# Kernel optimization log

Hardware: AMD Instinct MI355X
Metric: run time of the kernel (lower is better)

Reference implementation:

```python
import jax, jax.numpy as jnp
import numpy as np

N, E = 100000, 1600000
IN, H, ED, L, OUT = 128, 64, 64, 3, 3

def _lin(key, fan_in, fan_out):
    return jax.random.normal(key, (fan_in, fan_out), jnp.float32) / np.sqrt(fan_in)

def setup_inputs() -> dict:
    key = jax.random.key(0)
    ks = jax.random.split(key, 16)
    x = jax.random.normal(ks[0], (N, IN), jnp.float32)
    edge_index = jax.random.randint(ks[1], (2, E), 0, N, dtype=jnp.int64)
    edge_attr = jax.random.normal(ks[2], (E, ED), jnp.float32)
    pW = _lin(ks[3], IN, H); pb = jnp.zeros((H,), jnp.float32)
    # stacked per-layer params
    eW1 = jnp.stack([_lin(jax.random.fold_in(ks[4], l), 2 * H + ED, ED) for l in range(L)])
    eb1 = jnp.zeros((L, ED), jnp.float32)
    eW2 = jnp.stack([_lin(jax.random.fold_in(ks[5], l), ED, ED) for l in range(L)])
    eb2 = jnp.zeros((L, ED), jnp.float32)
    nW1 = jnp.stack([_lin(jax.random.fold_in(ks[6], l), H + ED, H) for l in range(L)])
    nb1 = jnp.zeros((L, H), jnp.float32)
    nW2 = jnp.stack([_lin(jax.random.fold_in(ks[7], l), H, H) for l in range(L)])
    nb2 = jnp.zeros((L, H), jnp.float32)
    lW = _lin(ks[8], H, OUT); lb = jnp.zeros((OUT,), jnp.float32)
    return {"x": x, "edge_index": edge_index, "edge_attr": edge_attr,
            "pW": pW, "pb": pb, "eW1": eW1, "eb1": eb1, "eW2": eW2, "eb2": eb2,
            "nW1": nW1, "nb1": nb1, "nW2": nW2, "nb2": nb2, "lW": lW, "lb": lb}

def reference(x, edge_index, edge_attr, pW, pb, eW1, eb1, eW2, eb2, nW1, nb1, nW2, nb2, lW, lb):
    n = x.shape[0]
    row, col = edge_index[0], edge_index[1]  # source j, target i
    h = x @ pW + pb                          # node_proj
    ea = edge_attr
    for l in range(eW1.shape[0]):
        # edge_mlp([x_row, x_col, e])
        ein = jnp.concatenate([h[row], h[col], ea], axis=-1)        # [E, 2H+ED]
        ea = jax.nn.relu(ein @ eW1[l] + eb1[l]) @ eW2[l] + eb2[l]   # [E, ED]
        # message = node_mlp([x_j, e]) with x_j = h[row]
        mi = jnp.concatenate([h[row], ea], axis=-1)                 # [E, H+ED]
        msg = jax.nn.relu(mi @ nW1[l] + nb1[l]) @ nW2[l] + nb2[l]   # [E, H]
        agg = jax.ops.segment_sum(msg, col, num_segments=n)         # scatter-add into targets
        h = jax.nn.relu(agg + h)                                    # update + outer ReLU (dropout=eval)
    pooled = jnp.mean(h, axis=0, keepdims=True)                     # global_mean_pool, single graph
    return pooled @ lW + lb
```

## Files before the change

### kernel.cpp

```cpp
#include <hip/hip_runtime.h>

#define NN 100000
#define NE 1600000
#define BINS_PAD 100352

typedef short s8v __attribute__((ext_vector_type(8)));
typedef float f32x4 __attribute__((ext_vector_type(4)));
typedef unsigned short u16;

__device__ __forceinline__ u16 f2bf(float f) {
    union { float f; unsigned u; } v; v.f = f;
    unsigned r = v.u + 0x7FFFu + ((v.u >> 16) & 1u);
    return (u16)(r >> 16);
}
__device__ __forceinline__ unsigned pk2(float a, float b) {
    return (unsigned)f2bf(a) | ((unsigned)f2bf(b) << 16);
}

__global__ void pack_weights(const float* __restrict__ pW,
                             const float* __restrict__ eW1, const float* __restrict__ eW2,
                             const float* __restrict__ nW1, const float* __restrict__ nW2,
                             u16* __restrict__ wpack) {
    int b = blockIdx.x, L = threadIdx.x;
    const float* src; int s, t;
    if (b < 16) { src = pW; s = b >> 2; t = b & 3; }
    else {
        int bb = b - 16, l = bb / 56, r = bb % 56;
        if (r < 24)      {            src = eW1 + l*192*64; s = r>>2; t = r&3; }
        else if (r < 32) { r -= 24;   src = eW2 + l*64*64;  s = r>>2; t = r&3; }
        else if (r < 48) { r -= 32;   src = nW1 + l*128*64; s = r>>2; t = r&3; }
        else             { r -= 48;   src = nW2 + l*64*64;  s = r>>2; t = r&3; }
    }
    int kbase = s*32 + (L>>4)*8;
    int n = t*16 + (L&15);
    u16* dst = wpack + (size_t)b*512 + (size_t)L*8;
#pragma unroll
    for (int j = 0; j < 8; ++j) dst[j] = f2bf(src[(kbase+j)*64 + n]);
}

__global__ void k_hist(const int* __restrict__ ei, int* __restrict__ hist) {
    int e = blockIdx.x * 256 + threadIdx.x;
    atomicAdd(&hist[ei[(size_t)NE + e]], 1);
}

__global__ void k_scan1(const int* __restrict__ hist, int* __restrict__ cursor,
                        int* __restrict__ blockSums) {
    __shared__ int sS[256];
    int t = threadIdx.x, b = blockIdx.x;
    int base = b*1024 + t*4;
    int v0 = hist[base], v1 = hist[base+1], v2 = hist[base+2], v3 = hist[base+3];
    int s4 = v0 + v1 + v2 + v3;
    sS[t] = s4; __syncthreads();
    for (int off = 1; off < 256; off <<= 1) {
        int x = (t >= off) ? sS[t-off] : 0;
        __syncthreads();
        sS[t] += x;
        __syncthreads();
    }
    int excl = sS[t] - s4;
    cursor[base] = excl; cursor[base+1] = excl+v0;
    cursor[base+2] = excl+v0+v1; cursor[base+3] = excl+v0+v1+v2;
    if (t == 255) blockSums[b] = sS[255];
}

__global__ void k_scan2(int* __restrict__ blockSums) {
    __shared__ int sS[128];
    int t = threadIdx.x;
    int v = (t < 98) ? blockSums[t] : 0;
    sS[t] = v; __syncthreads();
    for (int off = 1; off < 128; off <<= 1) {
        int x = (t >= off) ? sS[t-off] : 0;
        __syncthreads();
        sS[t] += x;
        __syncthreads();
    }
    if (t < 98) blockSums[t] = sS[t] - v;
}

__global__ void k_scan3(int* __restrict__ cursor, const int* __restrict__ blockSums) {
    int i = blockIdx.x*1024 + threadIdx.x*4;
    int add = blockSums[blockIdx.x];
    cursor[i] += add; cursor[i+1] += add; cursor[i+2] += add; cursor[i+3] += add;
}

__global__ void k_scatter(const int* __restrict__ ei, int* __restrict__ cursor,
                          int* __restrict__ rowP, int* __restrict__ colP,
                          int* __restrict__ pos) {
    int e = blockIdx.x * 256 + threadIdx.x;
    int c = ei[(size_t)NE + e];
    int p = atomicAdd(&cursor[c], 1);
    rowP[p] = ei[e];
    colP[p] = c;
    pos[e] = p;
}

__global__ void k_permute_ea(const float* __restrict__ ea, const int* __restrict__ pos,
                             u16* __restrict__ eaP) {
    int g = threadIdx.x >> 6, lane = threadIdx.x & 63;
    int e = blockIdx.x * 4 + g;
    int p = pos[e];
    eaP[(size_t)p*64 + lane] = f2bf(ea[(size_t)e*64 + lane]);
}

__global__ __launch_bounds__(256) void node_proj(const float* __restrict__ x,
                                                 const float* __restrict__ pb,
                                                 const u16* __restrict__ wpack,
                                                 float* __restrict__ h,
                                                 u16* __restrict__ h_bf) {
    __shared__ __align__(16) u16 sX[64*136];
    const int tid = threadIdx.x;
    const int n0 = blockIdx.x * 64;
    for (int i = tid; i < 64*32; i += 256) {
        int node = i >> 5, c = i & 31;
        float4 v = make_float4(0.f, 0.f, 0.f, 0.f);
        if (n0 + node < NN) v = *(const float4*)(x + (size_t)(n0+node)*128 + c*4);
        *(uint2*)&sX[node*136 + c*4] = make_uint2(pk2(v.x, v.y), pk2(v.z, v.w));
    }
    __syncthreads();
    const int w = tid >> 6, L = tid & 63;
    const int m = L & 15, kc = L >> 4;
    const int wb = w * 16;
    const f32x4 z = {0.f, 0.f, 0.f, 0.f};
    f32x4 acc[4] = {z, z, z, z};
#pragma unroll
    for (int s = 0; s < 4; ++s) {
        s8v a = *(const s8v*)&sX[(wb+m)*136 + s*32 + kc*8];
#pragma unroll
        for (int t = 0; t < 4; ++t) {
            s8v bf = *(const s8v*)(wpack + ((size_t)(s*4+t)*64 + L)*8);
            acc[t] = __builtin_amdgcn_mfma_f32_16x16x32_bf16(a, bf, acc[t], 0, 0, 0);
        }
    }
#pragma unroll
    for (int t = 0; t < 4; ++t) {
        int u = t*16 + m;
        float bias = pb[u];
#pragma unroll
        for (int r = 0; r < 4; ++r) {
            int node = n0 + wb + kc*4 + r;
            if (node < NN) {
                float v = acc[t][r] + bias;
                h[(size_t)node*64 + u] = v;
                h_bf[(size_t)node*64 + u] = f2bf(v);
            }
        }
    }
}

__global__ __launch_bounds__(256, 4) void edge_layer(const int* __restrict__ rowP,
                                                     const int* __restrict__ colP,
                                                     const u16* __restrict__ h_bf,
                                                     u16* __restrict__ ea_bf,
                                                     const u16* __restrict__ wp,
                                                     const float* __restrict__ eb1,
                                                     const float* __restrict__ eb2,
                                                     const float* __restrict__ nb1,
                                                     const float* __restrict__ nb2,
                                                     float* __restrict__ agg) {
    __shared__ __align__(16) u16 sB[4*32*136];
    __shared__ int sColP[128];
    __shared__ int sSeg[130];
    __shared__ int sCnt0, sK;
    float* msg = (float*)sB;
    const int tid = threadIdx.x;
    const int w = tid >> 6, L = tid & 63;
    const int m = L & 15, kc = L >> 4;
    const int wb = w * 32;
    const size_t e0 = (size_t)blockIdx.x * 128;
    u16* sW = sB + w * 32 * 136;

    if (tid < 128) sColP[tid] = colP[e0 + tid];
    __syncthreads();
    bool st = false;
    if (tid < 128) st = (tid == 0) || (sColP[tid] != sColP[tid-1]);
    unsigned long long mask = __ballot(st);
    if (tid == 0) sCnt0 = __popcll(mask);
    __syncthreads();
    if (st) {
        int base = (tid >= 64) ? sCnt0 : 0;
        int idx = base + __popcll(mask & ((1ull << (tid & 63)) - 1ull));
        sSeg[idx] = tid;
    }
    if (tid == 64) { int k = sCnt0 + __popcll(mask); sK = k; sSeg[k] = 128; }

    float be1[4], be2[4], bn1[4], bn2[4];
#pragma unroll
    for (int t = 0; t < 4; ++t) {
        int u = t*16 + m;
        be1[t] = eb1[u]; be2[t] = eb2[u]; bn1[t] = nb1[u]; bn2[t] = nb2[u];
    }
    int rowI[2], colI[2];
#pragma unroll
    for (int g = 0; g < 2; ++g) {
        rowI[g] = rowP[e0 + wb + g*16 + m];
        colI[g] = sColP[wb + g*16 + m];
    }

    const f32x4 z = {0.f, 0.f, 0.f, 0.f};
    f32x4 acc[2][4];

#pragma unroll
    for (int g = 0; g < 2; ++g)
#pragma unroll
        for (int t = 0; t < 4; ++t) acc[g][t] = z;
#pragma unroll
    for (int s = 0; s < 6; ++s) {
        s8v a[2];
#pragma unroll
        for (int g = 0; g < 2; ++g) {
            if (s < 2)
                a[g] = *(const s8v*)(h_bf + (size_t)rowI[g]*64 + s*32 + kc*8);
            else if (s < 4)
                a[g] = *(const s8v*)(h_bf + (size_t)colI[g]*64 + (s-2)*32 + kc*8);
            else
                a[g] = *(const s8v*)(ea_bf + (e0 + wb + g*16 + m)*64 + (s-4)*32 + kc*8);
        }
#pragma unroll
        for (int t = 0; t < 4; ++t) {
            s8v bf = *(const s8v*)(wp + ((size_t)(s*4+t)*64 + L)*8);
            acc[0][t] = __builtin_amdgcn_mfma_f32_16x16x32_bf16(a[0], bf, acc[0][t], 0, 0, 0);
            acc[1][t] = __builtin_amdgcn_mfma_f32_16x16x32_bf16(a[1], bf, acc[1][t], 0, 0, 0);
        }
    }
#pragma unroll
    for (int g = 0; g < 2; ++g)
#pragma unroll
        for (int t = 0; t < 4; ++t) {
            int u = t*16 + m;
#pragma unroll
            for (int r = 0; r < 4; ++r) {
                float v = acc[g][t][r] + be1[t];
                v = v > 0.f ? v : 0.f;
                sW[(g*16 + kc*4 + r)*136 + u] = f2bf(v);
            }
        }

    const u16* wp2 = wp + 24*512;
#pragma unroll
    for (int g = 0; g < 2; ++g)
#pragma unroll
        for (int t = 0; t < 4; ++t) acc[g][t] = z;
#pragma unroll
    for (int s = 0; s < 2; ++s) {
        s8v a0 = *(const s8v*)&sW[(m)*136 + s*32 + kc*8];
        s8v a1 = *(const s8v*)&sW[(16 + m)*136 + s*32 + kc*8];
#pragma unroll
        for (int t = 0; t < 4; ++t) {
            s8v bf = *(const s8v*)(wp2 + ((size_t)(s*4+t)*64 + L)*8);
            acc[0][t] = __builtin_amdgcn_mfma_f32_16x16x32_bf16(a0, bf, acc[0][t], 0, 0, 0);
            acc[1][t] = __builtin_amdgcn_mfma_f32_16x16x32_bf16(a1, bf, acc[1][t], 0, 0, 0);
        }
    }
#pragma unroll
    for (int g = 0; g < 2; ++g)
#pragma unroll
        for (int t = 0; t < 4; ++t) {
            int u = t*16 + m;
#pragma unroll
            for (int r = 0; r < 4; ++r) {
                float v = acc[g][t][r] + be2[t];
                sW[(g*16 + kc*4 + r)*136 + 64 + u] = f2bf(v);
            }
        }

    const u16* wp3 = wp + 32*512;
#pragma unroll
    for (int g = 0; g < 2; ++g)
#pragma unroll
        for (int t = 0; t < 4; ++t) acc[g][t] = z;
#pragma unroll
    for (int s = 0; s < 4; ++s) {
        s8v a[2];
#pragma unroll
        for (int g = 0; g < 2; ++g) {
            if (s < 2) {
                a[g] = *(const s8v*)(h_bf + (size_t)rowI[g]*64 + s*32 + kc*8);
            } else {
                a[g] = *(const s8v*)&sW[(g*16 + m)*136 + 64 + (s-2)*32 + kc*8];
                *(s8v*)(ea_bf + (e0 + wb + g*16 + m)*64 + (s-2)*32 + kc*8) = a[g];
            }
        }
#pragma unroll
        for (int t = 0; t < 4; ++t) {
            s8v bf = *(const s8v*)(wp3 + ((size_t)(s*4+t)*64 + L)*8);
            acc[0][t] = __builtin_amdgcn_mfma_f32_16x16x32_bf16(a[0], bf, acc[0][t], 0, 0, 0);
            acc[1][t] = __builtin_amdgcn_mfma_f32_16x16x32_bf16(a[1], bf, acc[1][t], 0, 0, 0);
        }
    }
#pragma unroll
    for (int g = 0; g < 2; ++g)
#pragma unroll
        for (int t = 0; t < 4; ++t) {
            int u = t*16 + m;
#pragma unroll
            for (int r = 0; r < 4; ++r) {
                float v = acc[g][t][r] + bn1[t];
                v = v > 0.f ? v : 0.f;
                sW[(g*16 + kc*4 + r)*136 + u] = f2bf(v);
            }
        }

    const u16* wp4 = wp + 48*512;
#pragma unroll
    for (int g = 0; g < 2; ++g)
#pragma unroll
        for (int t = 0; t < 4; ++t) acc[g][t] = z;
#pragma unroll
    for (int s = 0; s < 2; ++s) {
        s8v a0 = *(const s8v*)&sW[(m)*136 + s*32 + kc*8];
        s8v a1 = *(const s8v*)&sW[(16 + m)*136 + s*32 + kc*8];
#pragma unroll
        for (int t = 0; t < 4; ++t) {
            s8v bf = *(const s8v*)(wp4 + ((size_t)(s*4+t)*64 + L)*8);
            acc[0][t] = __builtin_amdgcn_mfma_f32_16x16x32_bf16(a0, bf, acc[0][t], 0, 0, 0);
            acc[1][t] = __builtin_amdgcn_mfma_f32_16x16x32_bf16(a1, bf, acc[1][t], 0, 0, 0);
        }
    }

    __syncthreads();
#pragma unroll
    for (int g = 0; g < 2; ++g)
#pragma unroll
        for (int t = 0; t < 4; ++t) {
#pragma unroll
            for (int r = 0; r < 4; ++r) {
                int er = wb + g*16 + kc*4 + r;
                msg[er*66 + t*16 + m] = acc[g][t][r] + bn2[t];
            }
        }
    __syncthreads();

    int k = sK;
    for (int s = w; s < k; s += 4) {
        int beg = sSeg[s], end = sSeg[s+1];
        int node = sColP[beg];
        float sum = 0.f;
        for (int e = beg; e < end; ++e) sum += msg[e*66 + L];
        unsafeAtomicAdd(&agg[(size_t)node*64 + L], sum);
    }
}

__global__ void update_h(float* __restrict__ h, float* __restrict__ agg,
                         u16* __restrict__ h_bf, int zero_agg) {
    int i = (blockIdx.x * 256 + threadIdx.x) * 4;
    float4 a = *(const float4*)(agg + i);
    float4 hv = *(const float4*)(h + i);
    float4 v;
    v.x = fmaxf(a.x + hv.x, 0.f);
    v.y = fmaxf(a.y + hv.y, 0.f);
    v.z = fmaxf(a.z + hv.z, 0.f);
    v.w = fmaxf(a.w + hv.w, 0.f);
    *(float4*)(h + i) = v;
    *(uint2*)(h_bf + i) = make_uint2(pk2(v.x, v.y), pk2(v.z, v.w));
    if (zero_agg) *(float4*)(agg + i) = make_float4(0.f, 0.f, 0.f, 0.f);
}

__global__ void pool1(const float* __restrict__ h, float* __restrict__ pooled) {
    float acc = 0.f;
    const int stride = gridDim.x * 256;
    for (int i = blockIdx.x * 256 + threadIdx.x; i < NN*64; i += stride)
        acc += h[i];
    __shared__ float sp[256];
    sp[threadIdx.x] = acc;
    __syncthreads();
    if (threadIdx.x < 64) {
        float v = sp[threadIdx.x] + sp[threadIdx.x+64] + sp[threadIdx.x+128] + sp[threadIdx.x+192];
        unsafeAtomicAdd(&pooled[threadIdx.x], v);
    }
}

__global__ void pool2(const float* __restrict__ pooled, const float* __restrict__ lW,
                      const float* __restrict__ lb, float* __restrict__ out) {
    int k = threadIdx.x;
    float v = pooled[k] * (1.0f / NN);
#pragma unroll
    for (int o = 0; o < 3; ++o) {
        float p = v * lW[k*3 + o];
        for (int off = 32; off > 0; off >>= 1)
            p += __shfl_down(p, off);
        if (k == 0) out[o] = p + lb[o];
    }
}

extern "C" void kernel_launch(void* const* d_in, const int* in_sizes, int n_in,
                              void* d_out, int out_size, void* d_ws, size_t ws_size,
                              hipStream_t stream) {
    const float* x         = (const float*)d_in[0];
    const int*   ei        = (const int*)d_in[1];
    const float* edge_attr = (const float*)d_in[2];
    const float* pW        = (const float*)d_in[3];
    const float* pb        = (const float*)d_in[4];
    const float* eW1       = (const float*)d_in[5];
    const float* eb1       = (const float*)d_in[6];
    const float* eW2       = (const float*)d_in[7];
    const float* eb2       = (const float*)d_in[8];
    const float* nW1       = (const float*)d_in[9];
    const float* nb1       = (const float*)d_in[10];
    const float* nW2       = (const float*)d_in[11];
    const float* nb2       = (const float*)d_in[12];
    const float* lW        = (const float*)d_in[13];
    const float* lb        = (const float*)d_in[14];
    float* out = (float*)d_out;

    char* ws = (char*)d_ws;
    float* h     = (float*)(ws);
    float* agg   = (float*)(ws + 25600000);
    u16*   h_bf  = (u16*)  (ws + 51200000);
    u16*   eaP   = (u16*)  (ws + 64000000);
    u16*   wpack = (u16*)  (ws + 268800000);
    float* pooled= (float*)(ws + 268988416);
    int*   rowP  = (int*)  (ws + 268988672);
    int*   colP  = (int*)  (ws + 275388672);
    int* hist      = (int*)agg;
    int* cursor    = hist + BINS_PAD;
    int* blockSums = cursor + BINS_PAD;
    int* pos       = blockSums + 128;

    hipMemsetAsync(hist, 0, BINS_PAD*4, stream);
    k_hist<<<NE/256, 256, 0, stream>>>(ei, hist);
    k_scan1<<<98, 256, 0, stream>>>(hist, cursor, blockSums);
    k_scan2<<<1, 128, 0, stream>>>(blockSums);
    k_scan3<<<98, 256, 0, stream>>>(cursor, blockSums);
    k_scatter<<<NE/256, 256, 0, stream>>>(ei, cursor, rowP, colP, pos);
    k_permute_ea<<<NE/4, 256, 0, stream>>>(edge_attr, pos, eaP);

    pack_weights<<<184, 64, 0, stream>>>(pW, eW1, eW2, nW1, nW2, wpack);
    node_proj<<<(NN + 63)/64, 256, 0, stream>>>(x, pb, wpack, h, h_bf);

    hipMemsetAsync(agg, 0, (size_t)NN*64*4, stream);
    for (int l = 0; l < 3; ++l) {
        edge_layer<<<NE/128, 256, 0, stream>>>(rowP, colP, h_bf, eaP,
                                               wpack + (16 + l*56)*512,
                                               eb1 + l*64, eb2 + l*64, nb1 + l*64, nb2 + l*64,
                                               agg);
        update_h<<<NN*64/4/256, 256, 0, stream>>>(h, agg, h_bf, l < 2 ? 1 : 0);
    }
    hipMemsetAsync(pooled, 0, 64*4, stream);
    pool1<<<256, 256, 0, stream>>>(h, pooled);
    pool2<<<1, 64, 0, stream>>>(pooled, lW, lb, out);
}
```

Baseline: 1.731 ms.

## Reduce edge-layer messages in registers with wave shuffles and trim LDS and stores

The edge layer no longer stages messages in shared memory with block-wide segment discovery. Each wave finds its own target-node segments with ballot and shuffle, reduces the MFMA accumulators in registers, and issues the atomics directly. This shrinks the LDS tile stride so occupancy can rise to 6 blocks per SM. It also packs row and col indices into a single int2 array, vectorises the edge-attribute permutation, and skips the edge-attribute and bf16 h writes in the last layer. The cost is more atomics when a target node's edges span several waves, plus a serial per-segment loop inside each wave.

```diff
diff --git a/kernel.cpp b/kernel.cpp
--- a/kernel.cpp
+++ b/kernel.cpp
@@ -3,6 +3,7 @@
 #define NN 100000
 #define NE 1600000
 #define BINS_PAD 100352
+#define STR 72
 
 typedef short s8v __attribute__((ext_vector_type(8)));
 typedef float f32x4 __attribute__((ext_vector_type(4)));
@@ -84,22 +85,25 @@
 }
 
 __global__ void k_scatter(const int* __restrict__ ei, int* __restrict__ cursor,
-                          int* __restrict__ rowP, int* __restrict__ colP,
-                          int* __restrict__ pos) {
+                          int2* __restrict__ rcP, int* __restrict__ pos) {
     int e = blockIdx.x * 256 + threadIdx.x;
     int c = ei[(size_t)NE + e];
     int p = atomicAdd(&cursor[c], 1);
-    rowP[p] = ei[e];
-    colP[p] = c;
+    rcP[p] = make_int2(ei[e], c);
     pos[e] = p;
 }
 
 __global__ void k_permute_ea(const float* __restrict__ ea, const int* __restrict__ pos,
                              u16* __restrict__ eaP) {
-    int g = threadIdx.x >> 6, lane = threadIdx.x & 63;
-    int e = blockIdx.x * 4 + g;
+    size_t t = (size_t)blockIdx.x * 256 + threadIdx.x;
+    int e = (int)(t >> 3), q = (int)(t & 7);
     int p = pos[e];
-    eaP[(size_t)p*64 + lane] = f2bf(ea[(size_t)e*64 + lane]);
+    const float4* src = (const float4*)(ea + (size_t)e*64 + q*8);
+    float4 v0 = src[0], v1 = src[1];
+    uint4 o;
+    o.x = pk2(v0.x, v0.y); o.y = pk2(v0.z, v0.w);
+    o.z = pk2(v1.x, v1.y); o.w = pk2(v1.z, v1.w);
+    *(uint4*)(eaP + (size_t)p*64 + q*8) = o;
 }
 
 __global__ __launch_bounds__(256) void node_proj(const float* __restrict__ x,
@@ -147,8 +151,7 @@
     }
 }
 
-__global__ __launch_bounds__(256, 4) void edge_layer(const int* __restrict__ rowP,
-                                                     const int* __restrict__ colP,
+__global__ __launch_bounds__(256, 6) void edge_layer(const int2* __restrict__ rcP,
                                                      const u16* __restrict__ h_bf,
                                                      u16* __restrict__ ea_bf,
                                                      const u16* __restrict__ wp,
@@ -156,45 +159,32 @@
                                                      const float* __restrict__ eb2,
                                                      const float* __restrict__ nb1,
                                                      const float* __restrict__ nb2,
-                                                     float* __restrict__ agg) {
-    __shared__ __align__(16) u16 sB[4*32*136];
-    __shared__ int sColP[128];
-    __shared__ int sSeg[130];
-    __shared__ int sCnt0, sK;
-    float* msg = (float*)sB;
+                                                     float* __restrict__ agg,
+                                                     int save_ea) {
+    __shared__ __align__(16) u16 sB[4*32*STR];
     const int tid = threadIdx.x;
     const int w = tid >> 6, L = tid & 63;
     const int m = L & 15, kc = L >> 4;
     const int wb = w * 32;
     const size_t e0 = (size_t)blockIdx.x * 128;
-    u16* sW = sB + w * 32 * 136;
-
-    if (tid < 128) sColP[tid] = colP[e0 + tid];
-    __syncthreads();
-    bool st = false;
-    if (tid < 128) st = (tid == 0) || (sColP[tid] != sColP[tid-1]);
-    unsigned long long mask = __ballot(st);
-    if (tid == 0) sCnt0 = __popcll(mask);
-    __syncthreads();
-    if (st) {
-        int base = (tid >= 64) ? sCnt0 : 0;
-        int idx = base + __popcll(mask & ((1ull << (tid & 63)) - 1ull));
-        sSeg[idx] = tid;
-    }
-    if (tid == 64) { int k = sCnt0 + __popcll(mask); sK = k; sSeg[k] = 128; }
-
-    float be1[4], be2[4], bn1[4], bn2[4];
+    u16* sW = sB + w * 32 * STR;
+
+    int2 rc0 = rcP[e0 + wb + (L & 31)];
+    int lcol = rc0.y;
+    int rowI[2], colI[2];
+#pragma unroll
+    for (int g = 0; g < 2; ++g) {
+        rowI[g] = __shfl(rc0.x, g*16 + m);
+        colI[g] = __shfl(rc0.y, g*16 + m);
+    }
+
+    float be1[4], be2[4], bn1[4];
 #pragma unroll
     for (int t = 0; t < 4; ++t) {
         int u = t*16 + m;
-        be1[t] = eb1[u]; be2[t] = eb2[u]; bn1[t] = nb1[u]; bn2[t] = nb2[u];
-    }
-    int rowI[2], colI[2];
-#pragma unroll
-    for (int g = 0; g < 2; ++g) {
-        rowI[g] = rowP[e0 + wb + g*16 + m];
-        colI[g] = sColP[wb + g*16 + m];
-    }
+        be1[t] = eb1[u]; be2[t] = eb2[u]; bn1[t] = nb1[u];
+    }
+    float bn2L = nb2[L];
 
     const f32x4 z = {0.f, 0.f, 0.f, 0.f};
     f32x4 acc[2][4];
@@ -231,7 +221,7 @@
             for (int r = 0; r < 4; ++r) {
                 float v = acc[g][t][r] + be1[t];
                 v = v > 0.f ? v : 0.f;
-                sW[(g*16 + kc*4 + r)*136 + u] = f2bf(v);
+                sW[(g*16 + kc*4 + r)*STR + u] = f2bf(v);
             }
         }
 
@@ -242,8 +232,8 @@
         for (int t = 0; t < 4; ++t) acc[g][t] = z;
 #pragma unroll
     for (int s = 0; s < 2; ++s) {
-        s8v a0 = *(const s8v*)&sW[(m)*136 + s*32 + kc*8];
-        s8v a1 = *(const s8v*)&sW[(16 + m)*136 + s*32 + kc*8];
+        s8v a0 = *(const s8v*)&sW[(m)*STR + s*32 + kc*8];
+        s8v a1 = *(const s8v*)&sW[(16 + m)*STR + s*32 + kc*8];
 #pragma unroll
         for (int t = 0; t < 4; ++t) {
             s8v bf = *(const s8v*)(wp2 + ((size_t)(s*4+t)*64 + L)*8);
@@ -259,7 +249,7 @@
 #pragma unroll
             for (int r = 0; r < 4; ++r) {
                 float v = acc[g][t][r] + be2[t];
-                sW[(g*16 + kc*4 + r)*136 + 64 + u] = f2bf(v);
+                sW[(g*16 + kc*4 + r)*STR + u] = f2bf(v);
             }
         }
 
@@ -276,8 +266,9 @@
             if (s < 2) {
                 a[g] = *(const s8v*)(h_bf + (size_t)rowI[g]*64 + s*32 + kc*8);
             } else {
-                a[g] = *(const s8v*)&sW[(g*16 + m)*136 + 64 + (s-2)*32 + kc*8];
-                *(s8v*)(ea_bf + (e0 + wb + g*16 + m)*64 + (s-2)*32 + kc*8) = a[g];
+                a[g] = *(const s8v*)&sW[(g*16 + m)*STR + (s-2)*32 + kc*8];
+                if (save_ea)
+                    *(s8v*)(ea_bf + (e0 + wb + g*16 + m)*64 + (s-2)*32 + kc*8) = a[g];
             }
         }
 #pragma unroll
@@ -296,7 +287,7 @@
             for (int r = 0; r < 4; ++r) {
                 float v = acc[g][t][r] + bn1[t];
                 v = v > 0.f ? v : 0.f;
-                sW[(g*16 + kc*4 + r)*136 + u] = f2bf(v);
+                sW[(g*16 + kc*4 + r)*STR + u] = f2bf(v);
             }
         }
 
@@ -307,8 +298,8 @@
         for (int t = 0; t < 4; ++t) acc[g][t] = z;
 #pragma unroll
     for (int s = 0; s < 2; ++s) {
-        s8v a0 = *(const s8v*)&sW[(m)*136 + s*32 + kc*8];
-        s8v a1 = *(const s8v*)&sW[(16 + m)*136 + s*32 + kc*8];
+        s8v a0 = *(const s8v*)&sW[(m)*STR + s*32 + kc*8];
+        s8v a1 = *(const s8v*)&sW[(16 + m)*STR + s*32 + kc*8];
 #pragma unroll
         for (int t = 0; t < 4; ++t) {
             s8v bf = *(const s8v*)(wp4 + ((size_t)(s*4+t)*64 + L)*8);
@@ -317,31 +308,41 @@
         }
     }
 
-    __syncthreads();
-#pragma unroll
-    for (int g = 0; g < 2; ++g)
-#pragma unroll
-        for (int t = 0; t < 4; ++t) {
+    unsigned long long smask;
+    {
+        int prev = __shfl(lcol, (L + 63) & 63);
+        bool sstart = (L < 32) && ((L == 0) || (lcol != prev));
+        smask = __ballot(sstart);
+    }
+    while (smask) {
+        int beg = (int)__builtin_ctzll(smask);
+        smask &= smask - 1;
+        int end = smask ? (int)__builtin_ctzll(smask) : 32;
+        int node = __shfl(lcol, beg);
+        float r0 = 0.f, r1 = 0.f, r2 = 0.f, r3 = 0.f;
+#pragma unroll
+        for (int g = 0; g < 2; ++g)
 #pragma unroll
             for (int r = 0; r < 4; ++r) {
-                int er = wb + g*16 + kc*4 + r;
-                msg[er*66 + t*16 + m] = acc[g][t][r] + bn2[t];
-            }
-        }
-    __syncthreads();
-
-    int k = sK;
-    for (int s = w; s < k; s += 4) {
-        int beg = sSeg[s], end = sSeg[s+1];
-        int node = sColP[beg];
-        float sum = 0.f;
-        for (int e = beg; e < end; ++e) sum += msg[e*66 + L];
-        unsafeAtomicAdd(&agg[(size_t)node*64 + L], sum);
+                int le = g*16 + kc*4 + r;
+                bool in = (le >= beg) && (le < end);
+                r0 += in ? acc[g][0][r] : 0.f;
+                r1 += in ? acc[g][1][r] : 0.f;
+                r2 += in ? acc[g][2][r] : 0.f;
+                r3 += in ? acc[g][3][r] : 0.f;
+            }
+        r0 += __shfl_xor(r0, 16); r0 += __shfl_xor(r0, 32);
+        r1 += __shfl_xor(r1, 16); r1 += __shfl_xor(r1, 32);
+        r2 += __shfl_xor(r2, 16); r2 += __shfl_xor(r2, 32);
+        r3 += __shfl_xor(r3, 16); r3 += __shfl_xor(r3, 32);
+        float rv = (kc == 0) ? r0 : (kc == 1) ? r1 : (kc == 2) ? r2 : r3;
+        rv += (float)(end - beg) * bn2L;
+        unsafeAtomicAdd(&agg[(size_t)node*64 + L], rv);
     }
 }
 
 __global__ void update_h(float* __restrict__ h, float* __restrict__ agg,
-                         u16* __restrict__ h_bf, int zero_agg) {
+                         u16* __restrict__ h_bf, int zero_agg, int write_hbf) {
     int i = (blockIdx.x * 256 + threadIdx.x) * 4;
     float4 a = *(const float4*)(agg + i);
     float4 hv = *(const float4*)(h + i);
@@ -351,7 +352,7 @@
     v.z = fmaxf(a.z + hv.z, 0.f);
     v.w = fmaxf(a.w + hv.w, 0.f);
     *(float4*)(h + i) = v;
-    *(uint2*)(h_bf + i) = make_uint2(pk2(v.x, v.y), pk2(v.z, v.w));
+    if (write_hbf) *(uint2*)(h_bf + i) = make_uint2(pk2(v.x, v.y), pk2(v.z, v.w));
     if (zero_agg) *(float4*)(agg + i) = make_float4(0.f, 0.f, 0.f, 0.f);
 }
 
@@ -409,8 +410,7 @@
     u16*   eaP   = (u16*)  (ws + 64000000);
     u16*   wpack = (u16*)  (ws + 268800000);
     float* pooled= (float*)(ws + 268988416);
-    int*   rowP  = (int*)  (ws + 268988672);
-    int*   colP  = (int*)  (ws + 275388672);
+    int2*  rcP   = (int2*) (ws + 268988672);
     int* hist      = (int*)agg;
     int* cursor    = hist + BINS_PAD;
     int* blockSums = cursor + BINS_PAD;
@@ -421,19 +421,19 @@
     k_scan1<<<98, 256, 0, stream>>>(hist, cursor, blockSums);
     k_scan2<<<1, 128, 0, stream>>>(blockSums);
     k_scan3<<<98, 256, 0, stream>>>(cursor, blockSums);
-    k_scatter<<<NE/256, 256, 0, stream>>>(ei, cursor, rowP, colP, pos);
-    k_permute_ea<<<NE/4, 256, 0, stream>>>(edge_attr, pos, eaP);
+    k_scatter<<<NE/256, 256, 0, stream>>>(ei, cursor, rcP, pos);
+    k_permute_ea<<<NE*8/256, 256, 0, stream>>>(edge_attr, pos, eaP);
 
     pack_weights<<<184, 64, 0, stream>>>(pW, eW1, eW2, nW1, nW2, wpack);
     node_proj<<<(NN + 63)/64, 256, 0, stream>>>(x, pb, wpack, h, h_bf);
 
     hipMemsetAsync(agg, 0, (size_t)NN*64*4, stream);
     for (int l = 0; l < 3; ++l) {
-        edge_layer<<<NE/128, 256, 0, stream>>>(rowP, colP, h_bf, eaP,
+        edge_layer<<<NE/128, 256, 0, stream>>>(rcP, h_bf, eaP,
                                                wpack + (16 + l*56)*512,
                                                eb1 + l*64, eb2 + l*64, nb1 + l*64, nb2 + l*64,
-                                               agg);
-        update_h<<<NN*64/4/256, 256, 0, stream>>>(h, agg, h_bf, l < 2 ? 1 : 0);
+                                               agg, l < 2 ? 1 : 0);
+        update_h<<<NN*64/4/256, 256, 0, stream>>>(h, agg, h_bf, l < 2 ? 1 : 0, l < 2 ? 1 : 0);
     }
     hipMemsetAsync(pooled, 0, 64*4, stream);
     pool1<<<256, 256, 0, stream>>>(h, pooled);
```

After: 1.944 ms. 12.4% more time.
